# Kernel tuning notes

Hardware: AMD Instinct MI355X
Metric: run time of the kernel (lower is better)

The kernel has to match this reference:

```python
import jax, jax.numpy as jnp
import numpy as np

TOP_RATIO = 0.7
MIN_PATCHES = 128
RANDOM_RATIO = 0.1


def setup_inputs() -> dict:
    key = jax.random.key(0)
    k1, k2, k3, k4 = jax.random.split(key, 4)
    B, N, D, H = 4, 16384, 512, 256
    features = jax.random.normal(k1, (B, N, D), dtype=jnp.float32)
    W_V = jax.random.normal(k2, (D, H), dtype=jnp.float32) * (1.0 / np.sqrt(D))
    W_U = jax.random.normal(k3, (D, H), dtype=jnp.float32) * (1.0 / np.sqrt(D))
    w_att = jax.random.normal(k4, (H,), dtype=jnp.float32) * (1.0 / np.sqrt(H))
    return {
        "features": features,
        "W_V": W_V, "b_V": jnp.zeros((H,), jnp.float32),
        "W_U": W_U, "b_U": jnp.zeros((H,), jnp.float32),
        "w_att": w_att, "b_att": jnp.zeros((), jnp.float32),
    }


def reference(features, W_V, b_V, W_U, b_U, w_att, b_att):
    B, N, D = features.shape
    # gated attention scoring (dropout disabled: eval mode)
    a_V = jnp.tanh(features @ W_V + b_V)              # (B, N, H)
    a_U = jax.nn.sigmoid(features @ W_U + b_U)        # (B, N, H)
    raw = (a_V * a_U) @ w_att + b_att                 # (B, N)
    attn = jax.nn.softmax(raw, axis=-1)               # (B, N)

    # static selection sizes
    k = min(max(int(N * TOP_RATIO), MIN_PATCHES), N)  # 11468
    n_rand = max(int(k * RANDOM_RATIO), 1)            # 1146
    n_top = k - n_rand                                # 10322

    # batched top-k (softmax is monotone in raw, same indices as torch.topk(attn))
    _, top_idx = jax.lax.top_k(attn, n_top)           # (B, n_top)

    # remaining = indices not in top_idx, ascending; fixed count N - n_top
    mask = jnp.ones((B, N), bool).at[jnp.arange(B)[:, None], top_idx].set(False)
    remaining = jnp.argsort(~mask, axis=-1, stable=True)[:, : N - n_top]  # (B, N-n_top)

    # uniform random sample of n_rand remaining indices per batch element
    scores = jax.random.uniform(jax.random.key(42), (B, N - n_top))
    perm = jnp.argsort(scores, axis=-1)[:, :n_rand]   # random n_rand positions
    rand_idx = jnp.take_along_axis(remaining, perm, axis=-1)  # (B, n_rand)

    sel_idx = jnp.sort(jnp.concatenate([top_idx, rand_idx], axis=-1), axis=-1)  # (B, k)
    selected = jnp.take_along_axis(features, sel_idx[:, :, None], axis=1)       # (B, k, D)
    return selected, attn, sel_idx
```

## Files before the change

### kernel.cpp

```cpp
#include <hip/hip_runtime.h>
#include <stdint.h>

#define B 4
#define N 16384
#define D 512
#define H 256
#define NROWS (B * N)
#define K_SEL 11468
#define N_TOP 10322
#define N_RAND 1146
#define N_REM (N - N_TOP)
#define HALF_CNT ((B * N_REM) / 2)

typedef float f32x4 __attribute__((ext_vector_type(4)));
typedef _Float16 f16x8 __attribute__((ext_vector_type(8)));
typedef int i32x4 __attribute__((ext_vector_type(4)));

#define GLDS16(g, l)                                                    \
  __builtin_amdgcn_global_load_lds(                                     \
      (const __attribute__((address_space(1))) void*)(const void*)(g),  \
      (__attribute__((address_space(3))) void*)(void*)(l), 16, 0, 0)

#define SCHED0 __builtin_amdgcn_sched_barrier(0)
#define SBAR __builtin_amdgcn_s_barrier

__device__ __forceinline__ uint32_t f2key(float x) {
  uint32_t u = __float_as_uint(x);
  return u ^ ((u & 0x80000000u) ? 0xFFFFFFFFu : 0x80000000u);
}

__device__ __forceinline__ void threefry(uint32_t x0, uint32_t x1,
                                         uint32_t& o0, uint32_t& o1) {
  const uint32_t k0 = 0u, k1 = 42u;
  const uint32_t ks[3] = {k0, k1, k0 ^ k1 ^ 0x1BD11BDAu};
  x0 += ks[0];
  x1 += ks[1];
  const int R0[4] = {13, 15, 26, 6}, R1[4] = {17, 29, 16, 24};
#pragma unroll
  for (int i = 0; i < 5; ++i) {
    const int* R = (i & 1) ? R1 : R0;
#pragma unroll
    for (int jr = 0; jr < 4; ++jr) {
      x0 += x1;
      x1 = (x1 << R[jr]) | (x1 >> (32 - R[jr]));
      x1 ^= x0;
    }
    x0 += ks[(i + 1) % 3];
    x1 += ks[(i + 2) % 3] + (uint32_t)(i + 1);
  }
  o0 = x0;
  o1 = x1;
}

__device__ __forceinline__ void rand_body(const int b, int* __restrict__ psel,
                                          char* smem, const int t) {
  uint32_t* skey = reinterpret_cast<uint32_t*>(smem);
  uint32_t* hist = reinterpret_cast<uint32_t*>(smem + 24248);
  int* wr4 = reinterpret_cast<int*>(smem + 25272);
  uint32_t* shp = reinterpret_cast<uint32_t*>(smem + 25288);
  int* shrk = reinterpret_cast<int*>(smem + 25292);
  const int lane = t & 63, w4 = t >> 6;

  for (int p = t; p < N_REM; p += 256) {
    psel[b * N_REM + p] = 0;
    const int f = b * N_REM + p;
    uint32_t o0, o1, bits;
    if (f < HALF_CNT) {
      threefry((uint32_t)f, (uint32_t)(f + HALF_CNT), o0, o1);
      bits = o0;
    } else {
      threefry((uint32_t)(f - HALF_CNT), (uint32_t)f, o0, o1);
      bits = o1;
    }
    const float u = __uint_as_float((bits >> 9) | 0x3f800000u) - 1.0f;
    skey[p] = f2key(u);
  }
  __syncthreads();

  uint32_t prefix = 0;
  int rk = N_RAND;
  for (int pass = 3; pass >= 0; --pass) {
    const int sh = pass * 8;
    hist[t] = 0;
    __syncthreads();
    for (int p = t; p < N_REM; p += 256) {
      const uint32_t key = skey[p];
      if (pass == 3 || (key >> (sh + 8)) == (prefix >> (sh + 8)))
        atomicAdd(&hist[(key >> sh) & 255], 1u);
    }
    __syncthreads();
    const int h = (int)hist[t];
    int v = h;
#pragma unroll
    for (int off = 1; off < 64; off <<= 1) {
      const int u2 = __shfl_up(v, off, 64);
      if (lane >= off) v += u2;
    }
    if (lane == 63) wr4[w4] = v;
    __syncthreads();
    int add = 0;
    for (int i = 0; i < w4; ++i) add += wr4[i];
    const int incl = v + add, excl = incl - h;
    if (incl >= rk && excl < rk) {
      *shp = prefix | ((uint32_t)t << sh);
      *shrk = rk - excl;
    }
    __syncthreads();
    prefix = *shp;
    rk = *shrk;
    __syncthreads();
  }

  const int CH = 24;
  const int p0 = t * CH;
  const int pe = (p0 + CH < N_REM) ? p0 + CH : N_REM;
  int ce = 0;
  for (int p = p0; p < pe; ++p) ce += (skey[p] == prefix);
  int v = ce;
#pragma unroll
  for (int off = 1; off < 64; off <<= 1) {
    const int u2 = __shfl_up(v, off, 64);
    if (lane >= off) v += u2;
  }
  if (lane == 63) wr4[w4] = v;
  __syncthreads();
  if (t == 0) {
    int run = 0;
    for (int i = 0; i < 4; ++i) {
      const int a = wr4[i];
      wr4[i] = run;
      run += a;
    }
  }
  __syncthreads();
  int ge = wr4[w4] + v - ce;
  for (int p = p0; p < pe; ++p) {
    const uint32_t key = skey[p];
    const bool pick = (key < prefix) || (key == prefix && ge < rk);
    ge += (key == prefix);
    if (pick) psel[b * N_REM + p] = 1;
  }
}

__global__ __launch_bounds__(256) void prep_kernel(
    const float* __restrict__ WV, const float* __restrict__ WU,
    _Float16* __restrict__ wt_h, _Float16* __restrict__ wt_l,
    int* __restrict__ psel) {
  __shared__ __align__(16) char pmem[25296];
  if (blockIdx.x >= 64) {
    rand_body(blockIdx.x - 64, psel, pmem, threadIdx.x);
    return;
  }
  _Float16(*th)[65] = reinterpret_cast<_Float16(*)[65]>(pmem);
  _Float16(*tl)[65] = reinterpret_cast<_Float16(*)[65]>(pmem + 8320);
  const int kb = (blockIdx.x >> 3) * 64;
  const int nb = (blockIdx.x & 7) * 64;
  const int tx = threadIdx.x & 63;
  const int ty = threadIdx.x >> 6;
  const float* src = (nb < 256) ? WV : WU;
  const int nsrc = nb & 255;
#pragma unroll
  for (int i = 0; i < 16; ++i) {
    const int k = ty + i * 4;
    const float x = src[(size_t)(kb + k) * H + nsrc + tx];
    const _Float16 h = (_Float16)x;
    th[k][tx] = h;
    tl[k][tx] = (_Float16)(x - (float)h);
  }
  __syncthreads();
  const int n_local = threadIdx.x & 63;
  const int c2 = threadIdx.x >> 6;
  const int s_local = c2 >> 1, half = c2 & 1;
  const int n = nb + n_local;
  const int s = (kb >> 5) + s_local;
  const int klb = s_local * 32 + half * 16;
  const int j = (n < 256) ? n : n - 256;
  const int ch = j >> 7;
  const int nl = ((n < 256) ? 0 : 128) + (j & 127);
  const int swz = (nl >> 1) & 3;
  f16x8 vh0, vh1, vl0, vl1;
#pragma unroll
  for (int e = 0; e < 8; ++e) {
    vh0[e] = th[klb + e][n_local];
    vh1[e] = th[klb + 8 + e][n_local];
    vl0[e] = tl[klb + e][n_local];
    vl1[e] = tl[klb + 8 + e][n_local];
  }
  const size_t orow = (size_t)s * 16384 + (size_t)ch * 8192 + (size_t)nl * 32;
  *reinterpret_cast<f16x8*>(wt_h + orow + (((2 * half) ^ swz) * 8)) = vh0;
  *reinterpret_cast<f16x8*>(wt_h + orow + (((2 * half + 1) ^ swz) * 8)) = vh1;
  *reinterpret_cast<f16x8*>(wt_l + orow + (((2 * half) ^ swz) * 8)) = vl0;
  *reinterpret_cast<f16x8*>(wt_l + orow + (((2 * half + 1) ^ swz) * 8)) = vl1;
}

__global__ __launch_bounds__(512, 4) void score_kernel(
    const float* __restrict__ feat, const _Float16* __restrict__ wt_h,
    const _Float16* __restrict__ wt_l, const float* __restrict__ bV,
    const float* __restrict__ bU, const float* __restrict__ watt,
    float* __restrict__ rawp) {
  __shared__ _Float16 Ah[128 * 32];
  __shared__ _Float16 Al[128 * 32];
  __shared__ _Float16 Bh0[256 * 32];
  __shared__ _Float16 Bl0[256 * 32];
  __shared__ _Float16 Bh1[256 * 32];
  __shared__ _Float16 Bl1[256 * 32];
  float* red = reinterpret_cast<float*>(Ah);

  const int tid = threadIdx.x;
  const int lane = tid & 63;
  const int lc = lane & 15;
  const int lg = lane >> 4;
  const int w = __builtin_amdgcn_readfirstlane(tid >> 6);
  const int rg = w >> 2;
  const int cg = w & 3;
  const int bid = blockIdx.x;
  const int c = bid & 1;
  const int row0 = (bid >> 1) * 128;
  const int phase = (bid & 3) * 4;

  const int rA = tid >> 2;
  const int gA = tid & 3;
  const float* aG = feat + (size_t)(row0 + rA) * D + gA * 8;
  const int awOff = rA * 32 + ((gA ^ ((rA >> 1) & 3)) << 3);

  const _Float16* pbh = wt_h + (size_t)c * 8192 + (size_t)w * 1024 + lane * 8;
  const _Float16* pbl = wt_l + (size_t)c * 8192 + (size_t)w * 1024 + lane * 8;
  const int ldsB = w * 1024;

  const int rswz = (lc >> 1) & 3;
  int aoff[4], boff[4];
#pragma unroll
  for (int mt = 0; mt < 4; ++mt)
    aoff[mt] = (rg * 64 + mt * 16 + lc) * 32 + ((lg ^ rswz) << 3);
#pragma unroll
  for (int nt = 0; nt < 4; ++nt) {
    const int nl =
        ((nt < 2) ? cg * 32 + nt * 16 : 128 + cg * 32 + (nt - 2) * 16) + lc;
    boff[nt] = nl * 32 + ((lg ^ rswz) << 3);
  }

  f32x4 acc[4][4] = {};
  f32x4 a0, a1;

  a0 = *(const f32x4*)(aG + phase * 32);
  a1 = *(const f32x4*)(aG + phase * 32 + 4);
  GLDS16(pbh + phase * 16384, &Bh0[ldsB]);
  GLDS16(pbh + phase * 16384 + 512, &Bh0[ldsB + 512]);
  GLDS16(pbl + phase * 16384, &Bl0[ldsB]);
  GLDS16(pbl + phase * 16384 + 512, &Bl0[ldsB + 512]);
  {
    f16x8 ahw, alw;
#pragma unroll
    for (int e = 0; e < 8; ++e) {
      const float x = (e < 4) ? a0[e] : a1[e - 4];
      const _Float16 h = (_Float16)x;
      ahw[e] = h;
      alw[e] = (_Float16)(x - (float)h);
    }
    *(f16x8*)&Ah[awOff] = ahw;
    *(f16x8*)&Al[awOff] = alw;
  }
  SCHED0;
  asm volatile("s_waitcnt lgkmcnt(0)" ::: "memory");
  asm volatile("s_waitcnt vmcnt(0)" ::: "memory");
  SBAR();
  SCHED0;

#pragma unroll 1
  for (int i = 0; i < 16; ++i) {
    const int knxs = (phase + i + 1) & 15;
    _Float16* BhN = (i & 1) ? Bh0 : Bh1;
    _Float16* BlN = (i & 1) ? Bl0 : Bl1;
    const _Float16* BhC = (i & 1) ? Bh1 : Bh0;
    const _Float16* BlC = (i & 1) ? Bl1 : Bl0;

    GLDS16(pbh + knxs * 16384, &BhN[ldsB]);
    GLDS16(pbh + knxs * 16384 + 512, &BhN[ldsB + 512]);
    GLDS16(pbl + knxs * 16384, &BlN[ldsB]);
    GLDS16(pbl + knxs * 16384 + 512, &BlN[ldsB + 512]);
    a0 = *(const f32x4*)(aG + knxs * 32);
    a1 = *(const f32x4*)(aG + knxs * 32 + 4);
    SCHED0;

    f16x8 ah[4], al[4];
#pragma unroll
    for (int mt = 0; mt < 4; ++mt) {
      ah[mt] = *(const f16x8*)&Ah[aoff[mt]];
      al[mt] = *(const f16x8*)&Al[aoff[mt]];
    }
    __builtin_amdgcn_s_setprio(1);
#pragma unroll
    for (int nt = 0; nt < 4; ++nt) {
      const f16x8 bh = *(const f16x8*)&BhC[boff[nt]];
      const f16x8 bl = *(const f16x8*)&BlC[boff[nt]];
#pragma unroll
      for (int mt = 0; mt < 4; ++mt)
        acc[mt][nt] = __builtin_amdgcn_mfma_f32_16x16x32_f16(ah[mt], bh,
                                                             acc[mt][nt], 0, 0, 0);
#pragma unroll
      for (int mt = 0; mt < 4; ++mt)
        acc[mt][nt] = __builtin_amdgcn_mfma_f32_16x16x32_f16(ah[mt], bl,
                                                             acc[mt][nt], 0, 0, 0);
#pragma unroll
      for (int mt = 0; mt < 4; ++mt)
        acc[mt][nt] = __builtin_amdgcn_mfma_f32_16x16x32_f16(al[mt], bh,
                                                             acc[mt][nt], 0, 0, 0);
    }
    __builtin_amdgcn_s_setprio(0);

    f16x8 ahw, alw;
#pragma unroll
    for (int e = 0; e < 8; ++e) {
      const float x = (e < 4) ? a0[e] : a1[e - 4];
      const _Float16 h = (_Float16)x;
      ahw[e] = h;
      alw[e] = (_Float16)(x - (float)h);
    }
    SCHED0;
    SBAR();
    SCHED0;
    *(f16x8*)&Ah[awOff] = ahw;
    *(f16x8*)&Al[awOff] = alw;
    SCHED0;
    asm volatile("s_waitcnt lgkmcnt(0)" ::: "memory");
    asm volatile("s_waitcnt vmcnt(0)" ::: "memory");
    SBAR();
    SCHED0;
  }

#pragma unroll
  for (int mt = 0; mt < 4; ++mt) {
    float rs[4] = {0.f, 0.f, 0.f, 0.f};
#pragma unroll
    for (int nt = 0; nt < 2; ++nt) {
      const int j = c * 128 + cg * 32 + nt * 16 + lc;
      const float bv = bV[j], bu = bU[j], wa = watt[j];
#pragma unroll
      for (int rr = 0; rr < 4; ++rr) {
        const float cV = acc[mt][nt][rr] + bv;
        const float cU = acc[mt][nt + 2][rr] + bu;
        const float e2 = __expf(2.0f * cV);
        const float aV = 1.0f - 2.0f / (e2 + 1.0f);
        const float aU = 1.0f / (1.0f + __expf(-cU));
        rs[rr] += aV * aU * wa;
      }
    }
#pragma unroll
    for (int rr = 0; rr < 4; ++rr) {
      float v = rs[rr];
      v += __shfl_xor(v, 1, 16);
      v += __shfl_xor(v, 2, 16);
      v += __shfl_xor(v, 4, 16);
      v += __shfl_xor(v, 8, 16);
      if (lc == 0) red[(rg * 64 + mt * 16 + lg * 4 + rr) * 5 + cg] = v;
    }
  }
  __syncthreads();
  if (tid < 128)
    rawp[(size_t)c * NROWS + row0 + tid] = red[tid * 5 + 0] + red[tid * 5 + 1] +
                                           red[tid * 5 + 2] + red[tid * 5 + 3];
}

__device__ __forceinline__ int scan1024(int c, int* wred, int tid) {
  const int lane = tid & 63, w = tid >> 6;
  int v = c;
#pragma unroll
  for (int off = 1; off < 64; off <<= 1) {
    const int u = __shfl_up(v, off, 64);
    if (lane >= off) v += u;
  }
  if (lane == 63) wred[w] = v;
  __syncthreads();
  if (tid == 0) {
    int run = 0;
    for (int i = 0; i < 16; ++i) {
      const int a = wred[i];
      wred[i] = run;
      run += a;
    }
  }
  __syncthreads();
  const int res = wred[w] + v - c;
  __syncthreads();
  return res;
}

__global__ __launch_bounds__(1024) void select_kernel(
    const float* __restrict__ rawp, const int* __restrict__ psel,
    float* __restrict__ attn_out, int* __restrict__ sel_ws,
    float* __restrict__ out_selidx) {
  const int b = blockIdx.x, t = threadIdx.x;
  const int lane = t & 63, w = t >> 6;
  __shared__ float sraw[N];
  __shared__ int whist[16][256];
  __shared__ int ghist[256];
  __shared__ float fred[16];
  __shared__ int wred[16];
  __shared__ float shM, shS;
  __shared__ uint32_t sh_prefix;
  __shared__ int sh_rk;
  const float* r0 = rawp + (size_t)b * N;
  const float* r1 = rawp + (size_t)NROWS + b * N;

  float m = -3.0e38f;
  for (int i = 0; i < 16; ++i) {
    const int idx = t + i * 1024;
    const float v = r0[idx] + r1[idx];
    sraw[idx] = v;
    m = fmaxf(m, v);
  }
  for (int off = 32; off > 0; off >>= 1) m = fmaxf(m, __shfl_down(m, off, 64));
  if (lane == 0) fred[w] = m;
  __syncthreads();
  if (t == 0) {
    float mm = fred[0];
    for (int i = 1; i < 16; ++i) mm = fmaxf(mm, fred[i]);
    shM = mm;
  }
  __syncthreads();
  const float M = shM;

  float ex[16];
  float s = 0.f;
  for (int i = 0; i < 16; ++i) {
    ex[i] = expf(sraw[t + i * 1024] - M);
    s += ex[i];
  }
  for (int off = 32; off > 0; off >>= 1) s += __shfl_down(s, off, 64);
  if (lane == 0) fred[w] = s;
  __syncthreads();
  if (t == 0) {
    float ss = 0.f;
    for (int i = 0; i < 16; ++i) ss += fred[i];
    shS = ss;
  }
  __syncthreads();
  const float inv = 1.0f / shS;

  for (int i = 0; i < 16; ++i)
    attn_out[b * N + t + i * 1024] = ex[i] * inv;

  uint32_t prefix = 0;
  int rk = N_TOP;
  for (int pass = 3; pass >= 0; --pass) {
    const int sh = pass * 8;
#pragma unroll
    for (int q = 0; q < 4; ++q) whist[w][lane * 4 + q] = 0;
    __syncthreads();
    for (int i = 0; i < 16; ++i) {
      const uint32_t key = f2key(sraw[t + i * 1024]);
      if (pass == 3 || (key >> (sh + 8)) == (prefix >> (sh + 8)))
        atomicAdd(&whist[w][(key >> sh) & 255], 1);
    }
    __syncthreads();
    if (t < 256) {
      int tot = 0;
      for (int ww = 0; ww < 16; ++ww) tot += whist[ww][t];
      ghist[t] = tot;
    }
    __syncthreads();
    int vS = 0, hrev = 0;
    if (t < 256) {
      hrev = ghist[255 - t];
      vS = hrev;
#pragma unroll
      for (int off = 1; off < 64; off <<= 1) {
        const int u2 = __shfl_up(vS, off, 64);
        if (lane >= off) vS += u2;
      }
      if (lane == 63) wred[t >> 6] = vS;
    }
    __syncthreads();
    if (t < 256) {
      int add = 0;
      const int w4 = t >> 6;
      for (int i = 0; i < w4; ++i) add += wred[i];
      const int incl = vS + add, excl = incl - hrev;
      if (incl >= rk && excl < rk) {
        sh_prefix = prefix | ((uint32_t)(255 - t) << sh);
        sh_rk = rk - excl;
      }
    }
    __syncthreads();
    prefix = sh_prefix;
    rk = sh_rk;
    __syncthreads();
  }
  const uint32_t T = prefix;
  const int tieTake = rk;

  const int n0 = t * 16;
  int cgt = 0, ceq = 0;
  for (int i = 0; i < 16; ++i) {
    const uint32_t key = f2key(sraw[n0 + i]);
    cgt += (key > T);
    ceq += (key == T);
  }
  const int gbase = scan1024(cgt, wred, t);
  const int ebase = scan1024(ceq, wred, t);
  int grun = gbase, erun = ebase;
  unsigned selmask = 0;
  int csel = 0;
  for (int i = 0; i < 16; ++i) {
    const int n = n0 + i;
    const uint32_t key = f2key(sraw[n]);
    const bool gt = key > T, eq = key == T;
    const bool mem = gt || (eq && erun < tieTake);
    int sel;
    if (mem) {
      sel = 1;
    } else {
      const int members_before = grun + (erun < tieTake ? erun : tieTake);
      const int p = n - members_before;
      sel = psel[b * N_REM + p];
    }
    selmask |= (unsigned)sel << i;
    csel += sel;
    grun += gt;
    erun += eq;
  }
  int q = scan1024(csel, wred, t);
  for (int i = 0; i < 16; ++i) {
    if ((selmask >> i) & 1) {
      const int n = n0 + i;
      sel_ws[b * K_SEL + q] = n;
      out_selidx[b * K_SEL + q] = (float)n;
      ++q;
    }
  }
}

__global__ __launch_bounds__(256) void gather_kernel(
    const float* __restrict__ feat, const int* __restrict__ sel_ws,
    float* __restrict__ out_sel) {
  const int qa = blockIdx.x * 2 + (threadIdx.x >> 7);
  const int tl = threadIdx.x & 127;
  const int b = qa / K_SEL;
  const int n = sel_ws[qa];
  const float4* src =
      reinterpret_cast<const float4*>(feat + (size_t)(b * N + n) * D);
  float4* dst = reinterpret_cast<float4*>(out_sel + (size_t)qa * D);
  dst[tl] = src[tl];
}

extern "C" void kernel_launch(void* const* d_in, const int* in_sizes, int n_in,
                              void* d_out, int out_size, void* d_ws,
                              size_t ws_size, hipStream_t stream) {
  const float* feat = (const float*)d_in[0];
  const float* WV = (const float*)d_in[1];
  const float* bV = (const float*)d_in[2];
  const float* WU = (const float*)d_in[3];
  const float* bU = (const float*)d_in[4];
  const float* watt = (const float*)d_in[5];
  const float* batt = (const float*)d_in[6];
  (void)batt;

  float* out = (float*)d_out;
  float* out_selected = out;
  float* out_attn = out + (size_t)B * K_SEL * D;
  float* out_selidx = out_attn + (size_t)B * N;

  _Float16* wt_h = (_Float16*)d_ws;
  _Float16* wt_l = wt_h + 512 * 512;
  float* rawp = (float*)(wt_l + 512 * 512);
  int* psel = (int*)(rawp + 2 * NROWS);
  int* sel_ws = psel + B * N_REM;

  prep_kernel<<<68, 256, 0, stream>>>(WV, WU, wt_h, wt_l, psel);
  score_kernel<<<(NROWS / 128) * 2, 512, 0, stream>>>(feat, wt_h, wt_l, bV, bU,
                                                      watt, rawp);
  select_kernel<<<B, 1024, 0, stream>>>(rawp, psel, out_attn, sel_ws,
                                        out_selidx);
  gather_kernel<<<(B * K_SEL) / 2, 256, 0, stream>>>(feat, sel_ws,
                                                     out_selected);
}
```

Measured before the change: 345.4 us.

## Move softmax sum and top-16-bit radix histogram into a parallel pre-pass kernel

Adds a 128-block sumhist kernel that sums the two raw partials, builds a 65536-bin histogram over the upper 16 key bits with global atomics, and computes per-block exp sums. The 4-block select kernel then skips the max pass and two of its four radix passes, finding the 16-bit prefix by scanning the global histogram. The prep kernel gains blocks that zero the histogram and a rewritten weight-transpose store pattern. The softmax drops max-subtraction and uses __expf, so it can overflow for large raw values, and it adds a kernel launch plus global atomic contention.

Result: slower. 355.4 us (+2.9%).

```diff
diff --git a/kernel.cpp b/kernel.cpp
--- a/kernel.cpp
+++ b/kernel.cpp
@@ -145,8 +145,13 @@
 __global__ __launch_bounds__(256) void prep_kernel(
     const float* __restrict__ WV, const float* __restrict__ WU,
     _Float16* __restrict__ wt_h, _Float16* __restrict__ wt_l,
-    int* __restrict__ psel) {
+    int* __restrict__ psel, uint32_t* __restrict__ ghist16) {
   __shared__ __align__(16) char pmem[25296];
+  if (blockIdx.x >= 68) {
+    uint32_t* g = ghist16 + (size_t)(blockIdx.x - 68) * 4096;
+    for (int i = threadIdx.x; i < 4096; i += 256) g[i] = 0;
+    return;
+  }
   if (blockIdx.x >= 64) {
     rand_body(blockIdx.x - 64, psel, pmem, threadIdx.x);
     return;
@@ -168,29 +173,29 @@
     tl[k][tx] = (_Float16)(x - (float)h);
   }
   __syncthreads();
-  const int n_local = threadIdx.x & 63;
-  const int c2 = threadIdx.x >> 6;
-  const int s_local = c2 >> 1, half = c2 & 1;
-  const int n = nb + n_local;
-  const int s = (kb >> 5) + s_local;
-  const int klb = s_local * 32 + half * 16;
-  const int j = (n < 256) ? n : n - 256;
-  const int ch = j >> 7;
-  const int nl = ((n < 256) ? 0 : 128) + (j & 127);
-  const int swz = (nl >> 1) & 3;
-  f16x8 vh0, vh1, vl0, vl1;
-#pragma unroll
-  for (int e = 0; e < 8; ++e) {
-    vh0[e] = th[klb + e][n_local];
-    vh1[e] = th[klb + 8 + e][n_local];
-    vl0[e] = tl[klb + e][n_local];
-    vl1[e] = tl[klb + 8 + e][n_local];
-  }
-  const size_t orow = (size_t)s * 16384 + (size_t)ch * 8192 + (size_t)nl * 32;
-  *reinterpret_cast<f16x8*>(wt_h + orow + (((2 * half) ^ swz) * 8)) = vh0;
-  *reinterpret_cast<f16x8*>(wt_h + orow + (((2 * half + 1) ^ swz) * 8)) = vh1;
-  *reinterpret_cast<f16x8*>(wt_l + orow + (((2 * half) ^ swz) * 8)) = vl0;
-  *reinterpret_cast<f16x8*>(wt_l + orow + (((2 * half + 1) ^ swz) * 8)) = vl1;
+  const int r = threadIdx.x >> 7;
+  const int q = threadIdx.x & 127;
+  const int ch2 = (nb & 255) >> 7;
+  const int nlbase = ((nb < 256) ? 0 : 128) + (nb & 127);
+  const size_t base =
+      (size_t)((kb >> 5) + r) * 16384 + (size_t)ch2 * 8192 + (size_t)nlbase * 32;
+#pragma unroll
+  for (int u = 0; u < 2; ++u) {
+    const int gi = q * 2 + u;
+    const int slot = gi & 3;
+    const int nll = gi >> 2;
+    const int swz = (nll >> 1) & 3;
+    const int gsrc = slot ^ swz;
+    const int kb8 = r * 32 + gsrc * 8;
+    f16x8 vh, vl;
+#pragma unroll
+    for (int e = 0; e < 8; ++e) {
+      vh[e] = th[kb8 + e][nll];
+      vl[e] = tl[kb8 + e][nll];
+    }
+    *reinterpret_cast<f16x8*>(wt_h + base + (size_t)gi * 8) = vh;
+    *reinterpret_cast<f16x8*>(wt_l + base + (size_t)gi * 8) = vl;
+  }
 }
 
 __global__ __launch_bounds__(512, 4) void score_kernel(
@@ -361,6 +366,28 @@
                                            red[tid * 5 + 2] + red[tid * 5 + 3];
 }
 
+__global__ __launch_bounds__(512) void sumhist_kernel(
+    float* rawp, uint32_t* __restrict__ ghist16, float* __restrict__ gpart) {
+  const int bid = blockIdx.x;
+  const int b = bid >> 5;
+  const int blk = bid & 31;
+  const int idx = b * N + blk * 512 + threadIdx.x;
+  const float v = rawp[idx] + rawp[(size_t)NROWS + idx];
+  rawp[idx] = v;
+  atomicAdd(&ghist16[((size_t)b << 16) + (f2key(v) >> 16)], 1u);
+  float e = __expf(v);
+  for (int off = 32; off > 0; off >>= 1) e += __shfl_down(e, off, 64);
+  __shared__ float wsum[8];
+  const int lane = threadIdx.x & 63, wv = threadIdx.x >> 6;
+  if (lane == 0) wsum[wv] = e;
+  __syncthreads();
+  if (threadIdx.x == 0) {
+    float s = 0.f;
+    for (int i = 0; i < 8; ++i) s += wsum[i];
+    gpart[b * 32 + blk] = s;
+  }
+}
+
 __device__ __forceinline__ int scan1024(int c, int* wred, int tid) {
   const int lane = tid & 63, w = tid >> 6;
   int v = c;
@@ -387,6 +414,7 @@
 
 __global__ __launch_bounds__(1024) void select_kernel(
     const float* __restrict__ rawp, const int* __restrict__ psel,
+    const uint32_t* __restrict__ ghist16, const float* __restrict__ gpart,
     float* __restrict__ attn_out, int* __restrict__ sel_ws,
     float* __restrict__ out_selidx) {
   const int b = blockIdx.x, t = threadIdx.x;
@@ -394,62 +422,79 @@
   __shared__ float sraw[N];
   __shared__ int whist[16][256];
   __shared__ int ghist[256];
-  __shared__ float fred[16];
   __shared__ int wred[16];
-  __shared__ float shM, shS;
+  __shared__ float shS;
   __shared__ uint32_t sh_prefix;
   __shared__ int sh_rk;
   const float* r0 = rawp + (size_t)b * N;
-  const float* r1 = rawp + (size_t)NROWS + b * N;
-
-  float m = -3.0e38f;
+
+  if (t < 64) {
+    float s = (t < 32) ? gpart[b * 32 + t] : 0.0f;
+    for (int off = 32; off > 0; off >>= 1) s += __shfl_down(s, off, 64);
+    if (t == 0) shS = s;
+  }
+  __syncthreads();
+  const float inv = 1.0f / shS;
+
   for (int i = 0; i < 16; ++i) {
     const int idx = t + i * 1024;
-    const float v = r0[idx] + r1[idx];
+    const float v = r0[idx];
     sraw[idx] = v;
-    m = fmaxf(m, v);
-  }
-  for (int off = 32; off > 0; off >>= 1) m = fmaxf(m, __shfl_down(m, off, 64));
-  if (lane == 0) fred[w] = m;
-  __syncthreads();
-  if (t == 0) {
-    float mm = fred[0];
-    for (int i = 1; i < 16; ++i) mm = fmaxf(mm, fred[i]);
-    shM = mm;
-  }
-  __syncthreads();
-  const float M = shM;
-
-  float ex[16];
-  float s = 0.f;
-  for (int i = 0; i < 16; ++i) {
-    ex[i] = expf(sraw[t + i * 1024] - M);
-    s += ex[i];
-  }
-  for (int off = 32; off > 0; off >>= 1) s += __shfl_down(s, off, 64);
-  if (lane == 0) fred[w] = s;
-  __syncthreads();
-  if (t == 0) {
-    float ss = 0.f;
-    for (int i = 0; i < 16; ++i) ss += fred[i];
-    shS = ss;
-  }
-  __syncthreads();
-  const float inv = 1.0f / shS;
-
-  for (int i = 0; i < 16; ++i)
-    attn_out[b * N + t + i * 1024] = ex[i] * inv;
-
-  uint32_t prefix = 0;
-  int rk = N_TOP;
-  for (int pass = 3; pass >= 0; --pass) {
+    attn_out[b * N + idx] = __expf(v) * inv;
+  }
+
+  const uint32_t* hb = ghist16 + ((size_t)b << 16);
+  int qs[16];
+  int loc = 0;
+#pragma unroll
+  for (int qq = 0; qq < 16; ++qq) {
+    const i32x4 h4 = *reinterpret_cast<const i32x4*>(hb + (t << 6) + (qq << 2));
+    qs[qq] = h4[0] + h4[1] + h4[2] + h4[3];
+    loc += qs[qq];
+  }
+  const int excl2 = scan1024(loc, wred, t);
+  const int incl2 = excl2 + loc;
+  const int above_end = N - incl2;
+  if (above_end < N_TOP && (N - excl2) >= N_TOP) {
+    int run = above_end;
+    int fq = -1, rrun = 0;
+#pragma unroll
+    for (int qq = 15; qq >= 0; --qq) {
+      if (fq < 0) {
+        if (run + qs[qq] >= N_TOP) { fq = qq; rrun = run; }
+        else run += qs[qq];
+      }
+    }
+    const i32x4 h4 = *reinterpret_cast<const i32x4*>(hb + (t << 6) + (fq << 2));
+    int run2 = rrun;
+    int fj = -1;
+#pragma unroll
+    for (int jj = 3; jj >= 0; --jj) {
+      if (fj < 0) {
+        const int cb = h4[jj];
+        if (run2 + cb >= N_TOP) {
+          fj = jj;
+          sh_prefix = ((uint32_t)((t << 6) + (fq << 2) + jj)) << 16;
+          sh_rk = N_TOP - run2;
+        } else {
+          run2 += cb;
+        }
+      }
+    }
+  }
+  __syncthreads();
+  uint32_t prefix = sh_prefix;
+  int rk = sh_rk;
+  __syncthreads();
+
+  for (int pass = 1; pass >= 0; --pass) {
     const int sh = pass * 8;
 #pragma unroll
-    for (int q = 0; q < 4; ++q) whist[w][lane * 4 + q] = 0;
+    for (int qz = 0; qz < 4; ++qz) whist[w][lane * 4 + qz] = 0;
     __syncthreads();
     for (int i = 0; i < 16; ++i) {
       const uint32_t key = f2key(sraw[t + i * 1024]);
-      if (pass == 3 || (key >> (sh + 8)) == (prefix >> (sh + 8)))
+      if ((key >> (sh + 8)) == (prefix >> (sh + 8)))
         atomicAdd(&whist[w][(key >> sh) & 255], 1);
     }
     __syncthreads();
@@ -563,14 +608,17 @@
   _Float16* wt_h = (_Float16*)d_ws;
   _Float16* wt_l = wt_h + 512 * 512;
   float* rawp = (float*)(wt_l + 512 * 512);
-  int* psel = (int*)(rawp + 2 * NROWS);
+  uint32_t* ghist16 = (uint32_t*)(rawp + 2 * NROWS);
+  float* gpart = (float*)(ghist16 + 4 * 65536);
+  int* psel = (int*)(gpart + 128);
   int* sel_ws = psel + B * N_REM;
 
-  prep_kernel<<<68, 256, 0, stream>>>(WV, WU, wt_h, wt_l, psel);
+  prep_kernel<<<132, 256, 0, stream>>>(WV, WU, wt_h, wt_l, psel, ghist16);
   score_kernel<<<(NROWS / 128) * 2, 512, 0, stream>>>(feat, wt_h, wt_l, bV, bU,
                                                       watt, rawp);
-  select_kernel<<<B, 1024, 0, stream>>>(rawp, psel, out_attn, sel_ws,
-                                        out_selidx);
+  sumhist_kernel<<<128, 512, 0, stream>>>(rawp, ghist16, gpart);
+  select_kernel<<<B, 1024, 0, stream>>>(rawp, psel, ghist16, gpart, out_attn,
+                                        sel_ws, out_selidx);
   gather_kernel<<<(B * K_SEL) / 2, 256, 0, stream>>>(feat, sel_ws,
                                                      out_selected);
 }
```
